# Kernel tuning notes

Hardware: AMD Instinct MI355X
Metric: run time of the kernel (lower is better)

The kernel has to match this reference:

```python
import jax, jax.numpy as jnp
import numpy as np


def setup_inputs() -> dict:
    key = jax.random.key(0)
    ks = jax.random.split(key, 16)
    B, S, D, H = 32, 2048, 512, 512
    s = 1.0 / np.sqrt(H)
    inp = {
        "x": jax.random.normal(ks[0], (B, H), jnp.float32),
        "context": jax.random.normal(ks[1], (B, S, D), jnp.float32),
        "mask": jnp.zeros((B, S), jnp.bool_),  # False = valid position
        "Wi": jax.random.normal(ks[2], (H, H), jnp.float32) * s,
        "bi": jax.random.normal(ks[3], (H,), jnp.float32) * s,
        "Wc0": jax.random.normal(ks[4], (H, D), jnp.float32) * s,
        "bc0": jax.random.normal(ks[5], (H,), jnp.float32) * s,
        "Wc1": jax.random.normal(ks[6], (H, D), jnp.float32) * s,
        "bc1": jax.random.normal(ks[7], (H,), jnp.float32) * s,
        "Wc2": jax.random.normal(ks[8], (H, D), jnp.float32) * s,
        "bc2": jax.random.normal(ks[9], (H,), jnp.float32) * s,
        "Wc3": jax.random.normal(ks[10], (H, D), jnp.float32) * s,
        "bc3": jax.random.normal(ks[11], (H,), jnp.float32) * s,
        "V": jax.random.uniform(ks[12], (H,), jnp.float32, -s, s),
    }
    return inp


def reference(x, context, mask, Wi, bi, Wc0, bc0, Wc1, bc1, Wc2, bc2, Wc3, bc3, V):
    # mask: True = masked out in the original API; module flips it first.
    valid = ~mask  # [B, S], True = keep

    inp = (x @ Wi.T + bi)[:, :, None]  # [B, H, 1]

    def proj(W, b):
        # Conv1d(D, H, kernel=1) on context.permute(0,2,1) == token-wise GEMM
        return jnp.einsum("bsd,hd->bhs", context, W) + b[None, :, None]  # [B, H, S]

    ctx = jnp.concatenate(
        [proj(Wc0, bc0), proj(Wc1, bc1), proj(Wc2, bc2), proj(Wc3, bc3)], axis=2
    )  # [B, H, 4S]

    t = jnp.tanh(inp + ctx)                      # [B, H, 4S]
    att = jnp.einsum("h,bhs->bs", V, t)          # bmm(V[B,1,H], t).squeeze(1)
    att = 10.0 * jnp.tanh(att)                   # [B, 4S]

    valid4 = jnp.tile(valid, (1, 4))             # mask.repeat(1, 4)
    att = jnp.where(valid4, att, -jnp.inf)
    # torch.no_grad() around the masked fill detaches the rest of the graph
    att = jax.lax.stop_gradient(att)

    ans = jax.nn.softmax(att, axis=1)            # [B, 4S]
    p = jnp.max(ans, axis=1)
    indices = jnp.argmax(ans, axis=1)
    return indices[:, None], p[:, None], mask
```

## Files before the change

### kernel.cpp

```cpp
#include <hip/hip_runtime.h>
#include <math.h>

typedef __bf16 bf16x8 __attribute__((ext_vector_type(8)));
typedef float f32x4 __attribute__((ext_vector_type(4)));
typedef short short8v __attribute__((ext_vector_type(8)));

#define MARGIN 0.01f
#define NCAND 32

#define WAITL  do { asm volatile("s_waitcnt lgkmcnt(0)" ::: "memory"); __builtin_amdgcn_sched_barrier(0); } while (0)
#define WAITV0 do { asm volatile("s_waitcnt vmcnt(0)" ::: "memory"); __builtin_amdgcn_sched_barrier(0); } while (0)
#define BARR   do { __builtin_amdgcn_s_barrier(); __builtin_amdgcn_sched_barrier(0); } while (0)

__device__ __forceinline__ unsigned short f2bf(float f) {
  unsigned u = __float_as_uint(f);
  u += 0x7fffu + ((u >> 16) & 1u);
  return (unsigned short)(u >> 16);
}
__device__ __forceinline__ float tanh_fast(float x) {
  float e = __builtin_amdgcn_exp2f(x * 2.885390081777927f);
  return 1.f - 2.f * __builtin_amdgcn_rcpf(e + 1.f);
}
__device__ __forceinline__ float exp_fast(float x) {
  return __builtin_amdgcn_exp2f(x * 1.4426950408889634f);
}
__device__ __forceinline__ void gl_lds16(const void* g, void* l) {
  __builtin_amdgcn_global_load_lds(
      (const __attribute__((address_space(1))) unsigned int*)g,
      (__attribute__((address_space(3))) unsigned int*)l, 16, 0, 0);
}
__device__ __forceinline__ int cvt_pk_bf16(float lo, float hi) {
  int r;
  asm("v_cvt_pk_bf16_f32 %0, %1, %2" : "=v"(r) : "v"(lo), "v"(hi));
  return r;
}
__device__ __forceinline__ float dpp_row_reduce(float v) {
  int x;
  x = __builtin_amdgcn_update_dpp(0, __builtin_bit_cast(int, v), 0x118, 0xf, 0xf, true);
  v += __builtin_bit_cast(float, x);
  x = __builtin_amdgcn_update_dpp(0, __builtin_bit_cast(int, v), 0x114, 0xf, 0xf, true);
  v += __builtin_bit_cast(float, x);
  x = __builtin_amdgcn_update_dpp(0, __builtin_bit_cast(int, v), 0x112, 0xf, 0xf, true);
  v += __builtin_bit_cast(float, x);
  x = __builtin_amdgcn_update_dpp(0, __builtin_bit_cast(int, v), 0x111, 0xf, 0xf, true);
  v += __builtin_bit_cast(float, x);
  return v;
}

__global__ __launch_bounds__(256) void prep_small_k(
    const float* __restrict__ x, const float* __restrict__ Wi,
    const float* __restrict__ bi,
    const float* __restrict__ w0, const float* __restrict__ w1,
    const float* __restrict__ w2, const float* __restrict__ w3,
    short* __restrict__ Whi, float* __restrict__ inp) {
  int bid = blockIdx.x;
  if (bid < 512) {
    int gid = bid * 256 + threadIdx.x;
    int c = gid & 3, row = (gid >> 2) & 511, TK = gid >> 11;
    int TN = TK >> 4, KS = TK & 15;
    const float* w = (TN == 0) ? w0 : (TN == 1) ? w1 : (TN == 2) ? w2 : w3;
    const float* src = w + (size_t)row * 512 + KS * 32 + c * 8;
    float f[8];
    *(float4*)&f[0] = *(const float4*)(src);
    *(float4*)&f[4] = *(const float4*)(src + 4);
    short8v hv;
    #pragma unroll
    for (int i = 0; i < 8; ++i) hv[i] = (short)f2bf(f[i]);
    *(short8v*)(Whi + (size_t)gid * 8) = hv;
  } else {
    int gid = (bid - 512) * 256 + threadIdx.x;
    int b = gid >> 9, h = gid & 511;
    const float* xr = x + b * 512;
    const float* wr = Wi + h * 512;
    float acc = bi[h];
    #pragma unroll 4
    for (int k = 0; k < 512; k += 4) {
      float4 xv = *(const float4*)(xr + k);
      float4 wv = *(const float4*)(wr + k);
      acc += xv.x * wv.x + xv.y * wv.y + xv.z * wv.z + xv.w * wv.w;
    }
    inp[gid] = acc;
  }
}

__global__ __launch_bounds__(1024, 4) void gemm_att_k(
    const float* __restrict__ ctx, const short* __restrict__ Whi,
    const float* __restrict__ inp,
    const float* __restrict__ bc0, const float* __restrict__ bc1,
    const float* __restrict__ bc2, const float* __restrict__ bc3,
    const float* __restrict__ V, float* __restrict__ att) {
  __shared__ __align__(16) char smem[3][40960];

  const int t = threadIdx.x;
  int d = blockIdx.x + (blockIdx.y << 3);
  int work = (d & 7) * 256 + (d >> 3);
  int mt = work >> 2, nt = work & 3;
  int b = mt >> 4;
  const float* bc = (nt == 0) ? bc0 : (nt == 1) ? bc1 : (nt == 2) ? bc2 : bc3;

  const int ac = t >> 1, ah = t & 1;
  const int ar = ac >> 2, aq = ac & 3;
  const float* aSrc = ctx + ((size_t)mt * 128 + ar) * 512 + aq * 8 + ah * 4;
  const int aDstOff = ar * 32 + aq * 8 + ah * 4;

  auto loadA = [&](int tile) -> float4 { return *(const float4*)(aSrc + tile * 32); };
  auto writeA = [&](const float4& v, int slot) {
    int2 w;
    w.x = cvt_pk_bf16(v.x, v.y);
    w.y = cvt_pk_bf16(v.z, v.w);
    *(int2*)((short*)&smem[slot][0] + aDstOff) = w;
  };
  auto stageB = [&](int tile, int slot) {
    const short* gB = Whi + (((size_t)nt * 16 + tile) << 14) + t * 8;
    short* lB = (short*)&smem[slot][8192] + t * 8;
    gl_lds16(gB,        lB);
    gl_lds16(gB + 8192, lB + 8192);
  };

  f32x4 acc[4][4];
  #pragma unroll
  for (int i = 0; i < 4; ++i)
    #pragma unroll
    for (int j = 0; j < 4; ++j) acc[i][j] = (f32x4){0.f, 0.f, 0.f, 0.f};

  const int lane = t & 63, wid = t >> 6;
  const int wr = wid >> 3, wc = wid & 7;
  const int fr = lane & 15, fq = lane >> 4;
  const int abase = (wr * 64 + fr) * 32 + fq * 8;
  const int bbase = 8192 / 2 + (wc * 64 + fr) * 32 + fq * 8;

  {
    float4 a0 = loadA(0), a1 = loadA(1);
    stageB(0, 0); stageB(1, 1);
    WAITV0;
    writeA(a0, 0); writeA(a1, 1);
    WAITL;
  }
  BARR;

  #pragma unroll
  for (int tt = 0; tt < 16; ++tt) {
    const int slot = tt % 3;
    const short* As = (const short*)&smem[slot][0];
    float4 anext;
    if (tt < 14) { anext = loadA(tt + 2); stageB(tt + 2, (tt + 2) % 3); }
    bf16x8 a[4], bv[4];
    #pragma unroll
    for (int mi = 0; mi < 4; ++mi) a[mi] = *(const bf16x8*)(As + abase + mi * 512);
    #pragma unroll
    for (int ni = 0; ni < 4; ++ni) bv[ni] = *(const bf16x8*)(As + bbase + ni * 512);
    WAITL;
    __builtin_amdgcn_s_setprio(1);
    #pragma unroll
    for (int mi = 0; mi < 4; ++mi)
      #pragma unroll
      for (int ni = 0; ni < 4; ++ni)
        acc[mi][ni] = __builtin_amdgcn_mfma_f32_16x16x32_bf16(a[mi], bv[ni], acc[mi][ni], 0, 0, 0);
    __builtin_amdgcn_s_setprio(0);
    __builtin_amdgcn_sched_barrier(0);
    if (tt < 14) {
      WAITV0;
      writeA(anext, (tt + 2) % 3);
    }
    BARR;
  }

  float vV[4], vP[4];
  #pragma unroll
  for (int ni = 0; ni < 4; ++ni) {
    int j = wc * 64 + ni * 16 + fr;
    vV[ni] = V[j];
    vP[ni] = inp[b * 512 + j] + bc[j];
  }
  size_t abatt = (size_t)b * 8192 + (size_t)nt * 2048;
  #pragma unroll
  for (int mi = 0; mi < 4; ++mi) {
    #pragma unroll
    for (int r = 0; r < 4; ++r) {
      float sum = 0.f;
      #pragma unroll
      for (int ni = 0; ni < 4; ++ni)
        sum += vV[ni] * tanh_fast(vP[ni] + acc[mi][ni][r]);
      sum = dpp_row_reduce(sum);
      if (fr == 15) {
        int s2 = (mt & 15) * 128 + wr * 64 + mi * 16 + fq * 4 + r;
        atomicAdd(&att[abatt + s2], sum);
      }
    }
  }
}

__global__ __launch_bounds__(1024) void tail_k(const float* __restrict__ att,
    const unsigned char* __restrict__ mask, const float* __restrict__ ctx,
    const float* __restrict__ Wc0, const float* __restrict__ Wc1,
    const float* __restrict__ Wc2, const float* __restrict__ Wc3,
    const float* __restrict__ bc0, const float* __restrict__ bc1,
    const float* __restrict__ bc2, const float* __restrict__ bc3,
    const float* __restrict__ inp, const float* __restrict__ V,
    float* __restrict__ out) {
  int b = blockIdx.x, t = threadIdx.x;
  __shared__ float sred[1024];
  __shared__ float sctx[512];
  __shared__ int scnt;
  __shared__ int scand_j[NCAND];
  __shared__ float scand_a[NCAND];
  __shared__ float sexact[NCAND];

  if (t == 0) scnt = 0;
  float bm = -1e30f;
  for (int j = t; j < 8192; j += 1024) {
    if (mask[b * 2048 + (j & 2047)]) continue;
    bm = fmaxf(bm, att[(size_t)b * 8192 + j]);
  }
  sred[t] = bm;
  __syncthreads();
  for (int s2 = 512; s2 > 0; s2 >>= 1) {
    if (t < s2) sred[t] = fmaxf(sred[t], sred[t + s2]);
    __syncthreads();
  }
  float mx = sred[0];
  float Lref = 10.f * tanh_fast(mx);
  __syncthreads();
  float se = 0.f;
  for (int j = t; j < 8192; j += 1024) {
    if (mask[b * 2048 + (j & 2047)]) continue;
    float a = att[(size_t)b * 8192 + j];
    se += exp_fast(10.f * tanh_fast(a) - Lref);
    if (a >= mx - MARGIN) {
      int slot = atomicAdd(&scnt, 1);
      if (slot < NCAND) { scand_j[slot] = j; scand_a[slot] = a; }
    }
  }
  sred[t] = se;
  __syncthreads();
  for (int s2 = 512; s2 > 0; s2 >>= 1) {
    if (t < s2) sred[t] += sred[t + s2];
    __syncthreads();
  }
  float den = sred[0];
  int n = min(scnt, NCAND);
  for (int j = t; j < 2048; j += 1024)
    out[64 + b * 2048 + j] = mask[b * 2048 + j] ? 1.0f : 0.0f;
  for (int i = 0; i < n; ++i) {
    int jj = scand_j[i];
    int g = jj >> 11, s = jj & 2047;
    const float* W  = (g == 0) ? Wc0 : (g == 1) ? Wc1 : (g == 2) ? Wc2 : Wc3;
    const float* bc = (g == 0) ? bc0 : (g == 1) ? bc1 : (g == 2) ? bc2 : bc3;
    const float* cr = ctx + ((size_t)b * 2048 + s) * 512;
    __syncthreads();
    if (t < 512) sctx[t] = cr[t];
    __syncthreads();
    float total = 0.f;
    if (t < 512) {
      const float* wrp = W + (size_t)t * 512;
      float acc = 0.f;
      #pragma unroll 4
      for (int k = 0; k < 512; k += 4) {
        float4 wv = *(const float4*)(wrp + k);
        acc += wv.x * sctx[k] + wv.y * sctx[k + 1] + wv.z * sctx[k + 2] + wv.w * sctx[k + 3];
      }
      total = V[t] * tanhf(inp[b * 512 + t] + bc[t] + acc);
    }
    sred[t] = total;
    __syncthreads();
    for (int s2 = 512; s2 > 0; s2 >>= 1) {
      if (t < s2) sred[t] += sred[t + s2];
      __syncthreads();
    }
    if (t == 0) sexact[i] = sred[0];
  }
  __syncthreads();
  if (t == 0) {
    float dd = den, best = -1e30f;
    int bj = 0x7fffffff;
    for (int i = 0; i < n; ++i) {
      float e = sexact[i];
      int j = scand_j[i];
      dd += exp_fast(10.f * tanh_fast(e) - Lref) - exp_fast(10.f * tanh_fast(scand_a[i]) - Lref);
      if (e > best || (e == best && j < bj)) { best = e; bj = j; }
    }
    out[b] = (float)bj;
    out[32 + b] = exp_fast(10.f * tanh_fast(best) - Lref) / dd;
  }
}

extern "C" void kernel_launch(void* const* d_in, const int* in_sizes, int n_in,
                              void* d_out, int out_size, void* d_ws, size_t ws_size,
                              hipStream_t stream) {
  const float* x    = (const float*)d_in[0];
  const float* ctx  = (const float*)d_in[1];
  const unsigned char* mask = (const unsigned char*)d_in[2];
  const float* Wi   = (const float*)d_in[3];
  const float* bi   = (const float*)d_in[4];
  const float* Wc0  = (const float*)d_in[5];
  const float* bc0  = (const float*)d_in[6];
  const float* Wc1  = (const float*)d_in[7];
  const float* bc1  = (const float*)d_in[8];
  const float* Wc2  = (const float*)d_in[9];
  const float* bc2  = (const float*)d_in[10];
  const float* Wc3  = (const float*)d_in[11];
  const float* bc3  = (const float*)d_in[12];
  const float* V    = (const float*)d_in[13];
  float* out = (float*)d_out;

  float* inp = (float*)d_ws;
  float* att = inp + 16384;
  short* Whi = (short*)(att + 262144);

  hipMemsetAsync(att, 0, 262144 * sizeof(float), stream);
  prep_small_k<<<576, 256, 0, stream>>>(x, Wi, bi, Wc0, Wc1, Wc2, Wc3, Whi, inp);
  gemm_att_k<<<dim3(8, 256), 1024, 0, stream>>>(ctx, Whi,
      inp, bc0, bc1, bc2, bc3, V, att);
  tail_k<<<32, 1024, 0, stream>>>(att, mask, ctx, Wc0, Wc1, Wc2, Wc3,
      bc0, bc1, bc2, bc3, inp, V, out);
}
```

Measured before the change: 268.4 us.

## Pre-convert context to bf16 in a prep pass and stream it directly to LDS

Adds a prep pass that converts the whole fp32 context to bf16 into workspace. The GEMM kernel can then load A tiles with direct global-to-LDS transfers, using a double buffer instead of the triple buffer with register staging. The aim is to cut the GEMM's A-side global traffic and the VALU conversion work, which the four N-tiles currently repeat for each M-tile. In exchange it adds an extra full read and write of context (64 MB read, 32 MB written) and needs a large workspace. A fallback direct kernel is kept for when the workspace is too small.

```diff
diff --git a/kernel.cpp b/kernel.cpp
--- a/kernel.cpp
+++ b/kernel.cpp
@@ -28,11 +28,6 @@
   __builtin_amdgcn_global_load_lds(
       (const __attribute__((address_space(1))) unsigned int*)g,
       (__attribute__((address_space(3))) unsigned int*)l, 16, 0, 0);
-}
-__device__ __forceinline__ int cvt_pk_bf16(float lo, float hi) {
-  int r;
-  asm("v_cvt_pk_bf16_f32 %0, %1, %2" : "=v"(r) : "v"(lo), "v"(hi));
-  return r;
 }
 __device__ __forceinline__ float dpp_row_reduce(float v) {
   int x;
@@ -47,15 +42,25 @@
   return v;
 }
 
-__global__ __launch_bounds__(256) void prep_small_k(
-    const float* __restrict__ x, const float* __restrict__ Wi,
-    const float* __restrict__ bi,
+__global__ __launch_bounds__(256) void prep_all_k(
+    const float* __restrict__ ctx, const float* __restrict__ x,
+    const float* __restrict__ Wi, const float* __restrict__ bi,
     const float* __restrict__ w0, const float* __restrict__ w1,
     const float* __restrict__ w2, const float* __restrict__ w3,
-    short* __restrict__ Whi, float* __restrict__ inp) {
+    short* __restrict__ Cbf, short* __restrict__ Whi, float* __restrict__ inp,
+    int ctx_blocks) {
   int bid = blockIdx.x;
-  if (bid < 512) {
-    int gid = bid * 256 + threadIdx.x;
+  if (bid < ctx_blocks) {
+    size_t i = ((size_t)bid * 256 + threadIdx.x) * 8;
+    float f[8];
+    *(float4*)&f[0] = *(const float4*)(ctx + i);
+    *(float4*)&f[4] = *(const float4*)(ctx + i + 4);
+    short8v hv;
+    #pragma unroll
+    for (int j = 0; j < 8; ++j) hv[j] = (short)f2bf(f[j]);
+    *(short8v*)(Cbf + i) = hv;
+  } else if (bid < ctx_blocks + 512) {
+    int gid = (bid - ctx_blocks) * 256 + threadIdx.x;
     int c = gid & 3, row = (gid >> 2) & 511, TK = gid >> 11;
     int TN = TK >> 4, KS = TK & 15;
     const float* w = (TN == 0) ? w0 : (TN == 1) ? w1 : (TN == 2) ? w2 : w3;
@@ -65,10 +70,10 @@
     *(float4*)&f[4] = *(const float4*)(src + 4);
     short8v hv;
     #pragma unroll
-    for (int i = 0; i < 8; ++i) hv[i] = (short)f2bf(f[i]);
+    for (int j = 0; j < 8; ++j) hv[j] = (short)f2bf(f[j]);
     *(short8v*)(Whi + (size_t)gid * 8) = hv;
   } else {
-    int gid = (bid - 512) * 256 + threadIdx.x;
+    int gid = (bid - ctx_blocks - 512) * 256 + threadIdx.x;
     int b = gid >> 9, h = gid & 511;
     const float* xr = x + b * 512;
     const float* wr = Wi + h * 512;
@@ -84,51 +89,135 @@
 }
 
 __global__ __launch_bounds__(1024, 4) void gemm_att_k(
+    const short* __restrict__ Cbf, const short* __restrict__ Whi,
+    const float* __restrict__ inp,
+    const float* __restrict__ bc0, const float* __restrict__ bc1,
+    const float* __restrict__ bc2, const float* __restrict__ bc3,
+    const float* __restrict__ V, float* __restrict__ att) {
+  __shared__ __align__(16) short smem[2][20480];
+
+  const int t = threadIdx.x;
+  int d = blockIdx.x + (blockIdx.y << 3);
+  int work = (d & 7) * 256 + (d >> 3);
+  int mt = work >> 2, nt = work & 3;
+  int b = mt >> 4;
+  const float* bc = (nt == 0) ? bc0 : (nt == 1) ? bc1 : (nt == 2) ? bc2 : bc3;
+
+  const short* aSrc = Cbf + ((size_t)(mt * 128 + (t >> 2))) * 512 + (t & 3) * 8;
+  auto stageA = [&](int tile, int slot) {
+    if (t < 512)
+      gl_lds16(aSrc + tile * 32, &smem[slot][t * 8]);
+  };
+  auto stageB = [&](int tile, int slot) {
+    const short* gB = Whi + (((size_t)nt * 16 + tile) << 14) + t * 8;
+    short* lB = &smem[slot][4096 + t * 8];
+    gl_lds16(gB,        lB);
+    gl_lds16(gB + 8192, lB + 8192);
+  };
+
+  f32x4 acc[4][4];
+  #pragma unroll
+  for (int i = 0; i < 4; ++i)
+    #pragma unroll
+    for (int j = 0; j < 4; ++j) acc[i][j] = (f32x4){0.f, 0.f, 0.f, 0.f};
+
+  const int lane = t & 63, wid = t >> 6;
+  const int wr = wid >> 3, wc = wid & 7;
+  const int fr = lane & 15, fq = lane >> 4;
+  const int abase = (wr * 64 + fr) * 32 + fq * 8;
+  const int bbase = 4096 + (wc * 64 + fr) * 32 + fq * 8;
+
+  stageA(0, 0); stageB(0, 0);
+  WAITV0;
+  BARR;
+
+  #pragma unroll 2
+  for (int tt = 0; tt < 16; ++tt) {
+    const int slot = tt & 1;
+    const short* s = &smem[slot][0];
+    bf16x8 a[4], bv[4];
+    #pragma unroll
+    for (int mi = 0; mi < 4; ++mi) a[mi] = *(const bf16x8*)(s + abase + mi * 512);
+    #pragma unroll
+    for (int ni = 0; ni < 4; ++ni) bv[ni] = *(const bf16x8*)(s + bbase + ni * 512);
+    if (tt < 15) { stageA(tt + 1, slot ^ 1); stageB(tt + 1, slot ^ 1); }
+    WAITL;
+    __builtin_amdgcn_s_setprio(1);
+    #pragma unroll
+    for (int mi = 0; mi < 4; ++mi)
+      #pragma unroll
+      for (int ni = 0; ni < 4; ++ni)
+        acc[mi][ni] = __builtin_amdgcn_mfma_f32_16x16x32_bf16(a[mi], bv[ni], acc[mi][ni], 0, 0, 0);
+    __builtin_amdgcn_s_setprio(0);
+    __builtin_amdgcn_sched_barrier(0);
+    if (tt < 15) { WAITV0; }
+    BARR;
+  }
+
+  float vV[4], vP[4];
+  #pragma unroll
+  for (int ni = 0; ni < 4; ++ni) {
+    int j = wc * 64 + ni * 16 + fr;
+    vV[ni] = V[j];
+    vP[ni] = inp[b * 512 + j] + bc[j];
+  }
+  size_t abatt = (size_t)b * 8192 + (size_t)nt * 2048;
+  #pragma unroll
+  for (int mi = 0; mi < 4; ++mi) {
+    #pragma unroll
+    for (int r = 0; r < 4; ++r) {
+      float sum = 0.f;
+      #pragma unroll
+      for (int ni = 0; ni < 4; ++ni)
+        sum += vV[ni] * tanh_fast(vP[ni] + acc[mi][ni][r]);
+      sum = dpp_row_reduce(sum);
+      if (fr == 15) {
+        int s2 = (mt & 15) * 128 + wr * 64 + mi * 16 + fq * 4 + r;
+        atomicAdd(&att[abatt + s2], sum);
+      }
+    }
+  }
+}
+
+__global__ __launch_bounds__(1024, 4) void gemm_direct_k(
     const float* __restrict__ ctx, const short* __restrict__ Whi,
     const float* __restrict__ inp,
     const float* __restrict__ bc0, const float* __restrict__ bc1,
     const float* __restrict__ bc2, const float* __restrict__ bc3,
     const float* __restrict__ V, float* __restrict__ att) {
   __shared__ __align__(16) char smem[3][40960];
-
   const int t = threadIdx.x;
   int d = blockIdx.x + (blockIdx.y << 3);
   int work = (d & 7) * 256 + (d >> 3);
   int mt = work >> 2, nt = work & 3;
   int b = mt >> 4;
   const float* bc = (nt == 0) ? bc0 : (nt == 1) ? bc1 : (nt == 2) ? bc2 : bc3;
-
   const int ac = t >> 1, ah = t & 1;
   const int ar = ac >> 2, aq = ac & 3;
   const float* aSrc = ctx + ((size_t)mt * 128 + ar) * 512 + aq * 8 + ah * 4;
   const int aDstOff = ar * 32 + aq * 8 + ah * 4;
-
   auto loadA = [&](int tile) -> float4 { return *(const float4*)(aSrc + tile * 32); };
   auto writeA = [&](const float4& v, int slot) {
-    int2 w;
-    w.x = cvt_pk_bf16(v.x, v.y);
-    w.y = cvt_pk_bf16(v.z, v.w);
-    *(int2*)((short*)&smem[slot][0] + aDstOff) = w;
+    short* dst = (short*)&smem[slot][0] + aDstOff;
+    dst[0] = (short)f2bf(v.x); dst[1] = (short)f2bf(v.y);
+    dst[2] = (short)f2bf(v.z); dst[3] = (short)f2bf(v.w);
   };
   auto stageB = [&](int tile, int slot) {
     const short* gB = Whi + (((size_t)nt * 16 + tile) << 14) + t * 8;
     short* lB = (short*)&smem[slot][8192] + t * 8;
-    gl_lds16(gB,        lB);
+    gl_lds16(gB, lB);
     gl_lds16(gB + 8192, lB + 8192);
   };
-
   f32x4 acc[4][4];
   #pragma unroll
   for (int i = 0; i < 4; ++i)
     #pragma unroll
     for (int j = 0; j < 4; ++j) acc[i][j] = (f32x4){0.f, 0.f, 0.f, 0.f};
-
   const int lane = t & 63, wid = t >> 6;
   const int wr = wid >> 3, wc = wid & 7;
   const int fr = lane & 15, fq = lane >> 4;
   const int abase = (wr * 64 + fr) * 32 + fq * 8;
-  const int bbase = 8192 / 2 + (wc * 64 + fr) * 32 + fq * 8;
-
+  const int bbase = 4096 + (wc * 64 + fr) * 32 + fq * 8;
   {
     float4 a0 = loadA(0), a1 = loadA(1);
     stageB(0, 0); stageB(1, 1);
@@ -137,8 +226,6 @@
     WAITL;
   }
   BARR;
-
-  #pragma unroll
   for (int tt = 0; tt < 16; ++tt) {
     const int slot = tt % 3;
     const short* As = (const short*)&smem[slot][0];
@@ -150,21 +237,15 @@
     #pragma unroll
     for (int ni = 0; ni < 4; ++ni) bv[ni] = *(const bf16x8*)(As + bbase + ni * 512);
     WAITL;
-    __builtin_amdgcn_s_setprio(1);
     #pragma unroll
     for (int mi = 0; mi < 4; ++mi)
       #pragma unroll
       for (int ni = 0; ni < 4; ++ni)
         acc[mi][ni] = __builtin_amdgcn_mfma_f32_16x16x32_bf16(a[mi], bv[ni], acc[mi][ni], 0, 0, 0);
-    __builtin_amdgcn_s_setprio(0);
     __builtin_amdgcn_sched_barrier(0);
-    if (tt < 14) {
-      WAITV0;
-      writeA(anext, (tt + 2) % 3);
-    }
+    if (tt < 14) { WAITV0; writeA(anext, (tt + 2) % 3); }
     BARR;
   }
-
   float vV[4], vP[4];
   #pragma unroll
   for (int ni = 0; ni < 4; ++ni) {
@@ -306,11 +387,22 @@
   float* inp = (float*)d_ws;
   float* att = inp + 16384;
   short* Whi = (short*)(att + 262144);
+  short* Cbf = Whi + 1048576;
+  size_t need = (size_t)((char*)(Cbf + 33554432) - (char*)d_ws);
+  bool packed = ws_size >= need;
 
   hipMemsetAsync(att, 0, 262144 * sizeof(float), stream);
-  prep_small_k<<<576, 256, 0, stream>>>(x, Wi, bi, Wc0, Wc1, Wc2, Wc3, Whi, inp);
-  gemm_att_k<<<dim3(8, 256), 1024, 0, stream>>>(ctx, Whi,
-      inp, bc0, bc1, bc2, bc3, V, att);
+  if (packed) {
+    prep_all_k<<<16960, 256, 0, stream>>>(ctx, x, Wi, bi,
+        Wc0, Wc1, Wc2, Wc3, Cbf, Whi, inp, 16384);
+    gemm_att_k<<<dim3(8, 256), 1024, 0, stream>>>(Cbf, Whi,
+        inp, bc0, bc1, bc2, bc3, V, att);
+  } else {
+    prep_all_k<<<576, 256, 0, stream>>>(ctx, x, Wi, bi,
+        Wc0, Wc1, Wc2, Wc3, nullptr, Whi, inp, 0);
+    gemm_direct_k<<<dim3(8, 256), 1024, 0, stream>>>(ctx, Whi,
+        inp, bc0, bc1, bc2, bc3, V, att);
+  }
   tail_k<<<32, 1024, 0, stream>>>(att, mask, ctx, Wc0, Wc1, Wc2, Wc3,
       bc0, bc1, bc2, bc3, inp, V, out);
 }
```

Result: slower. 303.4 us (+13.1%).
